# Optimization experiments

Measured on AMD Instinct MI355X. Metric: run time of the kernel, lower is better.

The kernel has to match this reference:

```python
import jax, jax.numpy as jnp
import numpy as np

N_S, N_G, D, K = 30000, 3000, 128, 16
SIGMA = 2.5
BOX = 60.0  # Angstrom box for random coordinates


def setup_inputs() -> dict:
    key = jax.random.key(0)
    ks = jax.random.split(key, 10)
    s = 1.0 / np.sqrt(D)
    return {
        'xs': jax.random.normal(ks[0], (N_S, D), jnp.float32),
        'xg': jax.random.normal(ks[1], (N_G, D), jnp.float32),
        'pos_s': jax.random.uniform(ks[2], (N_S, 3), jnp.float32) * BOX,
        'pos_g': jax.random.uniform(ks[3], (N_G, 3), jnp.float32) * BOX,
        'W_s_pre': jax.random.normal(ks[4], (D, D), jnp.float32) * s,
        'W_g_pre': jax.random.normal(ks[5], (D, D), jnp.float32) * s,
        'W_gs': jax.random.normal(ks[6], (D, D), jnp.float32) * s,
        'W_sg': jax.random.normal(ks[7], (D, D), jnp.float32) * s,
        'W_s_post': jax.random.normal(ks[8], (2 * D, D), jnp.float32) * s,
        'W_g_post': jax.random.normal(ks[9], (2 * D, D), jnp.float32) * s,
        'k': K,
    }


def reference(xs, xg, pos_s, pos_g, W_s_pre, W_g_pre, W_gs, W_sg, W_s_post, W_g_post, k):
    n_s, d = xs.shape
    # ---- compute_bipartite_graphs: knn of each graph node over surface nodes ----
    # squared pairwise distances via gemm form: (N_G, N_S)
    d2 = ((pos_g ** 2).sum(-1)[:, None] + (pos_s ** 2).sum(-1)[None, :]
          - 2.0 * pos_g @ pos_s.T)
    neg_d2, idx = jax.lax.top_k(-d2, k)          # idx: (N_G, K) surface neighbors
    w = jnp.exp(neg_d2 / (2.0 * SIGMA ** 2))     # RBF edge weight exp(-d^2/(2*sigma^2))
    # ---- pre blocks ----
    hs = xs @ W_s_pre                             # (N_S, D)
    hg = xg @ W_g_pre                             # (N_G, D)
    # ---- bp_gs block: graph -> surface weighted edge-conv (scatter-add) ----
    msg_gs = (hg @ W_gs)[:, None, :] * w[:, :, None]          # (N_G, K, D)
    xs_out = jnp.zeros((n_s, d), hs.dtype).at[idx.reshape(-1)].add(
        msg_gs.reshape(-1, d))
    # ---- bp_sg block: surface -> graph weighted edge-conv (gather-sum) ----
    xg_out = ((hs @ W_sg)[idx] * w[:, :, None]).sum(axis=1)   # (N_G, D)
    # ---- post blocks: combine pre features with message output ----
    xs_new = jax.nn.relu(jnp.concatenate([hs, xs_out], axis=-1) @ W_s_post)
    xg_new = jax.nn.relu(jnp.concatenate([hg, xg_out], axis=-1) @ W_g_post)
    return xs_new, xg_new
```

## Files before the change

### kernel.cpp

```cpp
#include <hip/hip_runtime.h>
#include <stdint.h>

#define N_S 30000
#define N_G 3000
#define DD  128
#define KK  16
#define NE  (N_G * KK)
#define NC  16
#define CELLS (NC * NC * NC)
#define CH  3.75f
#define CAP 16
#define SURV 192

#define FILL_BLOCKS 118
#define PACK_BLOCKS 384
#define KNN_BLOCKS  3000
#define NBS16 1875
#define NBG16 188
#define PRE_TILES (NBS16 + NBG16)
#define NBS 469
#define NBG 47
#define NTILE (NBS + NBG)

using v8s = __attribute__((ext_vector_type(8))) short;
using v4f = __attribute__((ext_vector_type(4))) float;

__device__ __forceinline__ float bf2f(unsigned short u) {
    union { unsigned int i; float f; } v; v.i = ((unsigned int)u) << 16; return v.f;
}
__device__ __forceinline__ unsigned short f2bf(float f) {
    union { float f; unsigned int i; } v; v.f = f;
    unsigned int x = v.i;
    return (unsigned short)((x + 0x7fffu + ((x >> 16) & 1u)) >> 16);
}
__device__ __forceinline__ float ldIn(const void* p, int i, int bf) {
    return bf ? bf2f(((const unsigned short*)p)[i]) : ((const float*)p)[i];
}
__device__ __forceinline__ void stOut(void* p, int i, float v, int bf) {
    if (bf) ((unsigned short*)p)[i] = f2bf(v);
    else    ((float*)p)[i] = v;
}
__device__ __forceinline__ int cellOf(float x) {
    int c = (int)(x * (1.0f / CH));
    if (c < 0) c = 0; if (c > NC - 1) c = NC - 1;
    return c;
}

__device__ __forceinline__ int detectFlag(const void* pos_g) {
    const unsigned int* w = (const unsigned int*)pos_g;
    int votes = 0;
#pragma unroll
    for (int i = 0; i < 16; ++i) {
        const unsigned int b = (w[i] >> 8) & 0xFFu;
        votes += (b >= 0x3Eu && b <= 0x42u) ? 1 : 0;
    }
    return votes >= 8;
}

__device__ bool knn_fast(int g, int bf, const void* pos_g,
                         const int* __restrict__ ccnt,
                         const float4* __restrict__ scell,
                         const float4* __restrict__ ovf, int novf,
                         int* __restrict__ idx_out, float* __restrict__ w_out,
                         double* skey, int* ssid)
{
    const int t = threadIdx.x;

    const float gxf = ldIn(pos_g, 3 * g + 0, bf);
    const float gyf = ldIn(pos_g, 3 * g + 1, bf);
    const float gzf = ldIn(pos_g, 3 * g + 2, bf);
    const double gx = (double)gxf, gy = (double)gyf, gz = (double)gzf;
    const int cx = cellOf(gxf), cy = cellOf(gyf), cz = cellOf(gzf);

    double m = 1e300;
    if (cx - 1 > 0)      { double d = gx - (double)(cx - 1) * 3.75; if (d < m) m = d; }
    if (cx + 1 < NC - 1) { double d = (double)(cx + 2) * 3.75 - gx; if (d < m) m = d; }
    if (cy - 1 > 0)      { double d = gy - (double)(cy - 1) * 3.75; if (d < m) m = d; }
    if (cy + 1 < NC - 1) { double d = (double)(cy + 2) * 3.75 - gy; if (d < m) m = d; }
    if (cz - 1 > 0)      { double d = gz - (double)(cz - 1) * 3.75; if (d < m) m = d; }
    if (cz + 1 < NC - 1) { double d = (double)(cz + 2) * 3.75 - gz; if (d < m) m = d; }
    if (m < 0.0) m = 0.0;
    const double m2eff = (m < 1e299) ? m * m * (1.0 - 1e-12) : 1e300;

    int cnt = 0, base = 0;
    if (t < 54) {
        const int cell = t >> 1, h = t & 1;
        const int dx = cell / 9 - 1, dy = (cell / 3) % 3 - 1, dz = cell % 3 - 1;
        const int X = cx + dx, Y = cy + dy, Z = cz + dz;
        if (X >= 0 && X < NC && Y >= 0 && Y < NC && Z >= 0 && Z < NC) {
            const int cid = (X * NC + Y) * NC + Z;
            int c = ccnt[cid]; if (c > CAP) c = CAP;
            const int lo = h * 8;
            const int hi = (c < lo + 8) ? c : (lo + 8);
            cnt = (hi > lo) ? (hi - lo) : 0;
            base = cid * CAP + lo;
        }
    }

    double d2v[8]; int sv[8]; bool okv[8];
#pragma unroll
    for (int i = 0; i < 8; ++i) {
        okv[i] = false; d2v[i] = 0.0; sv[i] = 0;
        if (i < cnt) {
            const float4 cd = scell[base + i];
            const double ddx = gx - (double)cd.x;
            const double ddy = gy - (double)cd.y;
            const double ddz = gz - (double)cd.z;
            const double d2 = ddx * ddx + ddy * ddy + ddz * ddz;
            if (d2 < m2eff) { okv[i] = true; d2v[i] = d2; sv[i] = __float_as_int(cd.w); }
        }
    }
    int myc = 0;
#pragma unroll
    for (int i = 0; i < 8; ++i) myc += okv[i] ? 1 : 0;

    int incl = myc;
    for (int d = 1; d < 64; d <<= 1) {
        int v = __shfl_up(incl, d);
        if (t >= d) incl += v;
    }
    int total = __shfl(incl, 63);
    int pos = incl - myc;
#pragma unroll
    for (int i = 0; i < 8; ++i) {
        if (okv[i]) {
            if (pos < SURV) { skey[pos] = d2v[i]; ssid[pos] = sv[i]; }
            ++pos;
        }
    }

    for (int i0 = 0; i0 < novf; i0 += 64) {
        const int i = i0 + t;
        bool act = (i < novf);
        double d2 = 0.0; int sidx = 0;
        if (act) {
            const float4 cd = ovf[i];
            const double ddx = gx - (double)cd.x;
            const double ddy = gy - (double)cd.y;
            const double ddz = gz - (double)cd.z;
            d2 = ddx * ddx + ddy * ddy + ddz * ddz;
            sidx = __float_as_int(cd.w);
            act = (d2 < m2eff);
        }
        const unsigned long long b = __ballot(act);
        const int p2 = total + (int)__popcll(b & ((1ull << t) - 1ull));
        if (act && p2 < SURV) { skey[p2] = d2; ssid[p2] = sidx; }
        total += (int)__popcll(b);
    }

    if (total < KK || total > SURV) return false;
    __syncthreads();

    const int n = total;
    double ki[3]; int si[3]; int rk[3]; int nv = 0;
    for (int i = t; i < n && nv < 3; i += 64) {
        ki[nv] = skey[i]; si[nv] = ssid[i]; rk[nv] = 0; ++nv;
    }
    for (int j = 0; j < n; ++j) {
        const double kj = skey[j]; const int sj = ssid[j];
#pragma unroll
        for (int q = 0; q < 3; ++q)
            if (q < nv)
                rk[q] += ((kj < ki[q]) || (kj == ki[q] && sj < si[q])) ? 1 : 0;
    }
#pragma unroll
    for (int q = 0; q < 3; ++q) {
        if (q < nv && rk[q] < KK) {
            idx_out[g * KK + rk[q]] = si[q];
            w_out[g * KK + rk[q]] = expf((float)(-ki[q]) * (1.0f / 12.5f));
        }
    }
    return true;
}

__device__ void knn_node(int g, int bf, const void* pos_g,
                         const int* __restrict__ ccnt,
                         const float4* __restrict__ scell,
                         const float4* __restrict__ ovf, int novf,
                         int* __restrict__ idx_out, float* __restrict__ w_out,
                         unsigned short* map16, int* s_base, int* s_pref,
                         double* g_key, int* g_sid)
{
    const int t = threadIdx.x;

    const float gxf = ldIn(pos_g, 3 * g + 0, bf);
    const float gyf = ldIn(pos_g, 3 * g + 1, bf);
    const float gzf = ldIn(pos_g, 3 * g + 2, bf);
    const double gx = (double)gxf, gy = (double)gyf, gz = (double)gzf;
    const int cx = cellOf(gxf), cy = cellOf(gyf), cz = cellOf(gzf);

    double bk[KK]; int bi[KK];
#pragma unroll
    for (int j = 0; j < KK; ++j) { bk[j] = 1e300; bi[j] = 0x7fffffff; }

    for (int i = t; i < novf; i += 64) {
        const float4 cd = ovf[i];
        const double ddx = gx - (double)cd.x, ddy = gy - (double)cd.y, ddz = gz - (double)cd.z;
        const double d2 = ddx * ddx + ddy * ddy + ddz * ddz;
        const int sidx = __float_as_int(cd.w);
        if (d2 > bk[KK - 1] || (d2 == bk[KK - 1] && sidx > bi[KK - 1])) continue;
        double ck = d2; int ci2 = sidx;
#pragma unroll
        for (int j = 0; j < KK; ++j) {
            const bool less = (ck < bk[j]) || (ck == bk[j] && ci2 < bi[j]);
            const double nk = less ? ck : bk[j]; const int ni = less ? ci2 : bi[j];
            const double ok = less ? bk[j] : ck; const int oi = less ? bi[j] : ci2;
            bk[j] = nk; bi[j] = ni; ck = ok; ci2 = oi;
        }
    }

    double gk15 = 1e300;
    for (int R = 1; R <= NC; ++R) {
        const int S = 2 * R + 1;
        const int Scells = S * S * S;
        for (int cb = 0; cb < Scells; cb += 64) {
            const int ci = cb + t;
            int cnt = 0, base = 0;
            if (ci < Scells) {
                const int dz = ci % S - R;
                const int dy = (ci / S) % S - R;
                const int dx = ci / (S * S) - R;
                int ax = dx < 0 ? -dx : dx, ay = dy < 0 ? -dy : dy, az = dz < 0 ? -dz : dz;
                int cheb = ax > ay ? ax : ay; if (az > cheb) cheb = az;
                const bool want = (R == 1) ? true : (cheb == R);
                const int X = cx + dx, Y = cy + dy, Z = cz + dz;
                if (want && X >= 0 && X < NC && Y >= 0 && Y < NC && Z >= 0 && Z < NC) {
                    double m2c = 0.0;
                    {
                        const double lo = (double)X * 3.75, hi = lo + 3.75;
                        const double d = (gx < lo) ? (lo - gx) : ((gx > hi) ? (gx - hi) : 0.0);
                        m2c += d * d;
                    }
                    {
                        const double lo = (double)Y * 3.75, hi = lo + 3.75;
                        const double d = (gy < lo) ? (lo - gy) : ((gy > hi) ? (gy - hi) : 0.0);
                        m2c += d * d;
                    }
                    {
                        const double lo = (double)Z * 3.75, hi = lo + 3.75;
                        const double d = (gz < lo) ? (lo - gz) : ((gz > hi) ? (gz - hi) : 0.0);
                        m2c += d * d;
                    }
                    if (m2c <= gk15 * (1.0 + 1e-9) + 1e-300) {
                        const int cid = (X * NC + Y) * NC + Z;
                        int c = ccnt[cid]; if (c > CAP) c = CAP;
                        cnt = c; base = cid * CAP;
                    }
                }
            }
            int incl = cnt;
            for (int d = 1; d < 64; d <<= 1) {
                int v = __shfl_up(incl, d);
                if (t >= d) incl += v;
            }
            const int total = __shfl(incl, 63);
            const int pref = incl - cnt;
            s_base[t] = base; s_pref[t] = pref;
            for (int i = 0; i < cnt; ++i) map16[pref + i] = (unsigned short)t;
            __syncthreads();
            for (int pos = t; pos < total; pos += 64) {
                const int slot = map16[pos];
                const float4 cd = scell[s_base[slot] + (pos - s_pref[slot])];
                const double ddx = gx - (double)cd.x;
                const double ddy = gy - (double)cd.y;
                const double ddz = gz - (double)cd.z;
                const double d2 = ddx * ddx + ddy * ddy + ddz * ddz;
                const int sidx = __float_as_int(cd.w);
                if (d2 > bk[KK - 1]) continue;
                if (d2 == bk[KK - 1] && sidx > bi[KK - 1]) continue;
                double ck = d2; int ci2 = sidx;
#pragma unroll
                for (int j = 0; j < KK; ++j) {
                    const bool less = (ck < bk[j]) || (ck == bk[j] && ci2 < bi[j]);
                    const double nk = less ? ck : bk[j]; const int ni = less ? ci2 : bi[j];
                    const double ok = less ? bk[j] : ck; const int oi = less ? bi[j] : ci2;
                    bk[j] = nk; bi[j] = ni; ck = ok; ci2 = oi;
                }
            }
            __syncthreads();
        }
        for (int p = 0; p < KK; ++p) {
            double key = bk[0]; int sid = bi[0];
            for (int d = 1; d < 64; d <<= 1) {
                const double ok = __shfl_xor(key, d);
                const int    os = __shfl_xor(sid, d);
                if (ok < key || (ok == key && os < sid)) { key = ok; sid = os; }
            }
            if (t == 0) { g_key[p] = key; g_sid[p] = sid; }
            const bool win = (bk[0] == key) && (bi[0] == sid);
            if (win) {
#pragma unroll
                for (int j = 0; j < KK - 1; ++j) { bk[j] = bk[j + 1]; bi[j] = bi[j + 1]; }
                bk[KK - 1] = 1e300; bi[KK - 1] = 0x7fffffff;
            }
        }
        __syncthreads();
        gk15 = g_key[KK - 1];
        if (t == 0) {
#pragma unroll
            for (int j = 0; j < KK; ++j) { bk[j] = g_key[j]; bi[j] = g_sid[j]; }
        } else {
#pragma unroll
            for (int j = 0; j < KK; ++j) { bk[j] = 1e300; bi[j] = 0x7fffffff; }
        }
        __syncthreads();
        double m = 1e300;
        if (cx - R > 0)      { double d = gx - (double)(cx - R) * 3.75; if (d < m) m = d; }
        if (cx + R < NC - 1) { double d = (double)(cx + R + 1) * 3.75 - gx; if (d < m) m = d; }
        if (cy - R > 0)      { double d = gy - (double)(cy - R) * 3.75; if (d < m) m = d; }
        if (cy + R < NC - 1) { double d = (double)(cy + R + 1) * 3.75 - gy; if (d < m) m = d; }
        if (cz - R > 0)      { double d = gz - (double)(cz - R) * 3.75; if (d < m) m = d; }
        if (cz + R < NC - 1) { double d = (double)(cz + R + 1) * 3.75 - gz; if (d < m) m = d; }
        if (m < 0.0) m = 0.0;
        const double m2 = m * m * (1.0 - 1e-12);
        if (gk15 < m2) break;
    }

    if (t == 0) {
        for (int p = 0; p < KK; ++p) {
            idx_out[g * KK + p] = g_sid[p];
            w_out[g * KK + p] = expf((float)(-g_key[p]) * (1.0f / 12.5f));
        }
    }
}

__device__ __forceinline__ v8s loadA_bf16(const unsigned short* p) {
    return *(const v8s*)p;
}
__device__ __forceinline__ v8s loadA_f32v(const float* f) {
    const float4 a = *(const float4*)f;
    const float4 b = *(const float4*)(f + 4);
    v8s r;
    r[0] = (short)f2bf(a.x); r[1] = (short)f2bf(a.y);
    r[2] = (short)f2bf(a.z); r[3] = (short)f2bf(a.w);
    r[4] = (short)f2bf(b.x); r[5] = (short)f2bf(b.y);
    r[6] = (short)f2bf(b.z); r[7] = (short)f2bf(b.w);
    return r;
}
__device__ __forceinline__ v8s loadA_raw(const void* A, size_t off, int bf) {
    if (bf) return loadA_bf16((const unsigned short*)A + off);
    return loadA_f32v((const float*)A + off);
}

__device__ void pre_tile16(int task, int bf, const void* xs, const void* xg,
                           const unsigned short* __restrict__ wpk_ps,
                           const unsigned short* __restrict__ wpk_pg,
                           unsigned short* __restrict__ hsb,
                           unsigned short* __restrict__ hgb,
                           float* __restrict__ xs_agg)
{
    const void* A; const unsigned short* wpk; unsigned short* outp; int M, m0;
    const bool is_s = (task < NBS16);
    if (is_s) { A = xs; wpk = wpk_ps; outp = hsb; M = N_S; m0 = task * 16; }
    else      { A = xg; wpk = wpk_pg; outp = hgb; M = N_G; m0 = (task - NBS16) * 16; }

    const int lane = threadIdx.x;
    const int q = lane >> 4, lm = lane & 15;
    const int mrow = m0 + lm;
    const bool valid = (mrow < M);

    v4f acc[8];
#pragma unroll
    for (int t = 0; t < 8; ++t) acc[t] = {0.f, 0.f, 0.f, 0.f};
    for (int ks = 0; ks < 4; ++ks) {
        v8s a = {0,0,0,0,0,0,0,0};
        if (valid) a = loadA_raw(A, (size_t)mrow * 128 + ks * 32 + q * 8, bf);
        const unsigned short* wb = wpk + (size_t)(ks * 4 + q) * 128 * 8;
#pragma unroll
        for (int t = 0; t < 8; ++t) {
            const v8s bfr = *(const v8s*)(wb + (t * 16 + lm) * 8);
            acc[t] = __builtin_amdgcn_mfma_f32_16x16x32_bf16(a, bfr, acc[t], 0, 0, 0);
        }
    }
#pragma unroll
    for (int t = 0; t < 8; ++t)
#pragma unroll
        for (int r = 0; r < 4; ++r) {
            const int row = m0 + q * 4 + r;
            if (row < M) outp[(size_t)row * 128 + t * 16 + lm] = f2bf(acc[t][r]);
        }
    if (is_s) {
        float4* dst = (float4*)(xs_agg + (size_t)m0 * 128);
        const float4 z = make_float4(0.f, 0.f, 0.f, 0.f);
        for (int i = lane; i < 16 * 32; i += 64) dst[i] = z;
    }
}

__device__ void post_tile(int task, int bf,
                          const unsigned short* __restrict__ hsb,
                          const float* __restrict__ xs_agg,
                          const unsigned short* __restrict__ hgb,
                          const unsigned short* __restrict__ aggg,
                          const unsigned short* __restrict__ wpk_cs,
                          const unsigned short* __restrict__ wpk_cg,
                          void* out)
{
    const unsigned short* A1; const void* A2; int a2f32; const unsigned short* wpk;
    int M, m0, ooff;
    if (task < NBS) { A1 = hsb; A2 = xs_agg; a2f32 = 1; wpk = wpk_cs; M = N_S; m0 = task * 64; ooff = 0; }
    else { A1 = hgb; A2 = aggg; a2f32 = 0; wpk = wpk_cg; M = N_G; m0 = (task - NBS) * 64; ooff = N_S * DD; }

    const int wave = threadIdx.x >> 6, lane = threadIdx.x & 63;
    const int q = lane >> 4, lm = lane & 15;
    const int mb = m0 + wave * 16;
    const int mrow = mb + lm;
    const bool valid = (mrow < M);

    v4f acc[8];
#pragma unroll
    for (int t = 0; t < 8; ++t) acc[t] = {0.f, 0.f, 0.f, 0.f};
    for (int ks = 0; ks < 8; ++ks) {
        const int kk = ks * 32 + q * 8;
        v8s a = {0,0,0,0,0,0,0,0};
        if (valid) {
            if (kk < 128)      a = loadA_bf16(A1 + (size_t)mrow * 128 + kk);
            else if (a2f32)    a = loadA_f32v((const float*)A2 + (size_t)mrow * 128 + (kk - 128));
            else               a = loadA_bf16((const unsigned short*)A2 + (size_t)mrow * 128 + (kk - 128));
        }
        const unsigned short* wb = wpk + (size_t)(ks * 4 + q) * 128 * 8;
#pragma unroll
        for (int t = 0; t < 8; ++t) {
            const v8s bfr = *(const v8s*)(wb + (t * 16 + lm) * 8);
            acc[t] = __builtin_amdgcn_mfma_f32_16x16x32_bf16(a, bfr, acc[t], 0, 0, 0);
        }
    }
#pragma unroll
    for (int t = 0; t < 8; ++t)
#pragma unroll
        for (int r = 0; r < 4; ++r) {
            const int row = mb + q * 4 + r;
            if (row < M) {
                float v = acc[t][r];
                if (v < 0.f) v = 0.f;
                stOut(out, ooff + row * DD + t * 16 + lm, v, bf);
            }
        }
}

__global__ __launch_bounds__(256) void fill_pack_kernel(
    const void* pos_s, const void* pos_g,
    const void* Wsp, const void* Wgp, const void* Wgs, const void* Wsg,
    const void* Wspost, const void* Wgpost,
    int* __restrict__ ccnt, float4* __restrict__ scell,
    float4* __restrict__ ovf, int* __restrict__ novf,
    unsigned short* __restrict__ wpk_ps, unsigned short* __restrict__ wpk_pg,
    unsigned short* __restrict__ wpk_cs, unsigned short* __restrict__ wpk_cg)
{
    const int bf = detectFlag(pos_g);
    const int bid = blockIdx.x, tid = threadIdx.x;
    if (bid < FILL_BLOCKS) {
        const int p = bid * 256 + tid;
        if (p < N_S) {
            const float x = ldIn(pos_s, 3 * p + 0, bf);
            const float y = ldIn(pos_s, 3 * p + 1, bf);
            const float z = ldIn(pos_s, 3 * p + 2, bf);
            const int cid = (cellOf(x) * NC + cellOf(y)) * NC + cellOf(z);
            const int slot = atomicAdd(&ccnt[cid], 1);
            const float4 pt = make_float4(x, y, z, __int_as_float(p));
            if (slot < CAP) scell[cid * CAP + slot] = pt;
            else            ovf[atomicAdd(novf, 1)] = pt;
        }
        return;
    }
    __shared__ float rows[256];
    const int rt = bid - FILL_BLOCKS;
    const int half = tid >> 7, j = tid & 127;
    const int task = rt * 2 + half;
    float v; unsigned short* dst; int k;
    if (task < 128) { k = task; v = ldIn(Wsp, k * DD + j, bf); dst = wpk_ps; }
    else if (task < 256) { k = task - 128; v = ldIn(Wgp, k * DD + j, bf); dst = wpk_pg; }
    else {
        const int which_g = (task >= 512);
        const int r = which_g ? (task - 512) : (task - 256);
        const void* W1 = which_g ? Wsg : Wgs;
        const void* Wp = which_g ? Wgpost : Wspost;
        dst = which_g ? wpk_cg : wpk_cs;
        k = r;
        if (r < 128) v = ldIn(Wp, r * DD + j, bf);
        else {
            rows[half * 128 + j] = ldIn(W1, (r - 128) * DD + j, bf);
            __syncthreads();
            float acc = 0.f;
            for (int m = 0; m < DD; ++m)
                acc += rows[half * 128 + m] * ldIn(Wp, (DD + m) * DD + j, bf);
            v = acc;
        }
    }
    const int ks = k >> 5, q = (k >> 3) & 3, i = k & 7;
    dst[((ks * 4 + q) * 128 + j) * 8 + i] = f2bf(v);
}

__global__ __launch_bounds__(64) void knn_pre_kernel(
    const void* xs, const void* xg, const void* pos_g,
    const int* __restrict__ ccnt, const float4* __restrict__ scell,
    const float4* __restrict__ ovf, const int* __restrict__ novf,
    int* __restrict__ idx, float* __restrict__ w,
    const unsigned short* __restrict__ wpk_ps,
    const unsigned short* __restrict__ wpk_pg,
    unsigned short* __restrict__ hsb, unsigned short* __restrict__ hgb,
    float* __restrict__ xs_agg)
{
    const int bf = detectFlag(pos_g);
    const int bid = blockIdx.x;
    if (bid < KNN_BLOCKS) {
        __shared__ double skey[SURV];
        __shared__ int    ssid[SURV];
        const int nov = *novf;
        if (!knn_fast(bid, bf, pos_g, ccnt, scell, ovf, nov, idx, w, skey, ssid)) {
            __shared__ unsigned short map16[64 * CAP];
            __shared__ int s_base[64];
            __shared__ int s_pref[64];
            __shared__ double g_key[KK];
            __shared__ int g_sid[KK];
            __syncthreads();
            knn_node(bid, bf, pos_g, ccnt, scell, ovf, nov, idx, w,
                     map16, s_base, s_pref, g_key, g_sid);
        }
    } else {
        pre_tile16(bid - KNN_BLOCKS, bf, xs, xg, wpk_ps, wpk_pg, hsb, hgb, xs_agg);
    }
}

__global__ __launch_bounds__(256) void scatgath_kernel(
    const unsigned short* __restrict__ hsb, const unsigned short* __restrict__ hgb,
    const int* __restrict__ idx, const float* __restrict__ w,
    float* __restrict__ xs_agg, unsigned short* __restrict__ aggg)
{
    const int g = blockIdx.x;
    const int half = threadIdx.x >> 7, j = threadIdx.x & 127;
    if (half == 0) {
        const float m = bf2f(hgb[g * DD + j]);
#pragma unroll
        for (int k = 0; k < KK; ++k)
            atomicAdd(&xs_agg[(size_t)idx[g * KK + k] * DD + j], m * w[g * KK + k]);
    } else {
        float acc = 0.f;
#pragma unroll
        for (int k = 0; k < KK; ++k)
            acc += w[g * KK + k] * bf2f(hsb[(size_t)idx[g * KK + k] * DD + j]);
        aggg[g * DD + j] = f2bf(acc);
    }
}

__global__ __launch_bounds__(256) void mfma_post_kernel(
    const void* pos_g,
    const unsigned short* __restrict__ hsb, const float* __restrict__ xs_agg,
    const unsigned short* __restrict__ hgb, const unsigned short* __restrict__ aggg,
    const unsigned short* __restrict__ wpk_cs, const unsigned short* __restrict__ wpk_cg,
    void* out)
{
    const int bf = detectFlag(pos_g);
    post_tile(blockIdx.x, bf, hsb, xs_agg, hgb, aggg, wpk_cs, wpk_cg, out);
}

extern "C" void kernel_launch(void* const* d_in, const int* in_sizes, int n_in,
                              void* d_out, int out_size, void* d_ws, size_t ws_size,
                              hipStream_t stream)
{
    const void* xs       = d_in[0];
    const void* xg       = d_in[1];
    const void* pos_s    = d_in[2];
    const void* pos_g    = d_in[3];
    const void* W_s_pre  = d_in[4];
    const void* W_g_pre  = d_in[5];
    const void* W_gs     = d_in[6];
    const void* W_sg     = d_in[7];
    const void* W_s_post = d_in[8];
    const void* W_g_post = d_in[9];
    (void)in_sizes; (void)n_in; (void)out_size; (void)ws_size;

    char* ws = (char*)d_ws;
    size_t off_b = 0;
    auto alloc = [&](size_t bytes) -> void* {
        void* p = ws + off_b;
        off_b = (off_b + bytes + 255) & ~((size_t)255);
        return p;
    };
    unsigned short* hsb    = (unsigned short*)alloc((size_t)N_S * DD * 2);
    unsigned short* hgb    = (unsigned short*)alloc((size_t)N_G * DD * 2);
    unsigned short* aggg   = (unsigned short*)alloc((size_t)N_G * DD * 2);
    float*          xs_agg = (float*) alloc((size_t)N_S * DD * 4);
    unsigned short* wpk_ps = (unsigned short*)alloc((size_t)DD * DD * 2);
    unsigned short* wpk_pg = (unsigned short*)alloc((size_t)DD * DD * 2);
    unsigned short* wpk_cs = (unsigned short*)alloc((size_t)2 * DD * DD * 2);
    unsigned short* wpk_cg = (unsigned short*)alloc((size_t)2 * DD * DD * 2);
    int*            idx    = (int*)   alloc((size_t)NE * 4);
    float*          w      = (float*) alloc((size_t)NE * 4);
    int*            ccnt   = (int*)   alloc((size_t)CELLS * 4 + 4);
    int*            novf   = ccnt + CELLS;
    float4*         scell  = (float4*)alloc((size_t)CELLS * CAP * 16);
    float4*         ovf    = (float4*)alloc((size_t)N_S * 16);

    hipMemsetAsync(ccnt, 0, (size_t)CELLS * 4 + 4, stream);

    fill_pack_kernel<<<FILL_BLOCKS + PACK_BLOCKS, 256, 0, stream>>>(
        pos_s, pos_g, W_s_pre, W_g_pre, W_gs, W_sg, W_s_post, W_g_post,
        ccnt, scell, ovf, novf, wpk_ps, wpk_pg, wpk_cs, wpk_cg);

    knn_pre_kernel<<<KNN_BLOCKS + PRE_TILES, 64, 0, stream>>>(
        xs, xg, pos_g, ccnt, scell, ovf, novf, idx, w,
        wpk_ps, wpk_pg, hsb, hgb, xs_agg);

    scatgath_kernel<<<N_G, 256, 0, stream>>>(hsb, hgb, idx, w,
                                             xs_agg, aggg);

    mfma_post_kernel<<<NTILE, 256, 0, stream>>>(pos_g, hsb, xs_agg, hgb, aggg,
                                                wpk_cs, wpk_cg, d_out);
}
```

Before: 186.7 us.

## Pack four waves per block for knn and pre tiles with expanding-region search

```diff
diff --git a/kernel.cpp b/kernel.cpp
--- a/kernel.cpp
+++ b/kernel.cpp
@@ -10,14 +10,15 @@
 #define CELLS (NC * NC * NC)
 #define CH  3.75f
 #define CAP 16
-#define SURV 192
+#define SURV 320
 
 #define FILL_BLOCKS 118
 #define PACK_BLOCKS 384
-#define KNN_BLOCKS  3000
+#define NODE_BLOCKS 750
 #define NBS16 1875
 #define NBG16 188
 #define PRE_TILES (NBS16 + NBG16)
+#define PRE_BLOCKS 516
 #define NBS 469
 #define NBG 47
 #define NTILE (NBS + NBG)
@@ -57,80 +58,86 @@
     return votes >= 8;
 }
 
-__device__ bool knn_fast(int g, int bf, const void* pos_g,
-                         const int* __restrict__ ccnt,
-                         const float4* __restrict__ scell,
-                         const float4* __restrict__ ovf, int novf,
-                         int* __restrict__ idx_out, float* __restrict__ w_out,
-                         double* skey, int* ssid)
-{
-    const int t = threadIdx.x;
-
-    const float gxf = ldIn(pos_g, 3 * g + 0, bf);
-    const float gyf = ldIn(pos_g, 3 * g + 1, bf);
-    const float gzf = ldIn(pos_g, 3 * g + 2, bf);
-    const double gx = (double)gxf, gy = (double)gyf, gz = (double)gzf;
-    const int cx = cellOf(gxf), cy = cellOf(gyf), cz = cellOf(gzf);
-
+__device__ __forceinline__ double regionM2(double gx, double gy, double gz,
+                                           int cx, int cy, int cz, int R)
+{
     double m = 1e300;
-    if (cx - 1 > 0)      { double d = gx - (double)(cx - 1) * 3.75; if (d < m) m = d; }
-    if (cx + 1 < NC - 1) { double d = (double)(cx + 2) * 3.75 - gx; if (d < m) m = d; }
-    if (cy - 1 > 0)      { double d = gy - (double)(cy - 1) * 3.75; if (d < m) m = d; }
-    if (cy + 1 < NC - 1) { double d = (double)(cy + 2) * 3.75 - gy; if (d < m) m = d; }
-    if (cz - 1 > 0)      { double d = gz - (double)(cz - 1) * 3.75; if (d < m) m = d; }
-    if (cz + 1 < NC - 1) { double d = (double)(cz + 2) * 3.75 - gz; if (d < m) m = d; }
+    if (cx - R > 0)      { double d = gx - (double)(cx - R) * 3.75; if (d < m) m = d; }
+    if (cx + R < NC - 1) { double d = (double)(cx + R + 1) * 3.75 - gx; if (d < m) m = d; }
+    if (cy - R > 0)      { double d = gy - (double)(cy - R) * 3.75; if (d < m) m = d; }
+    if (cy + R < NC - 1) { double d = (double)(cy + R + 1) * 3.75 - gy; if (d < m) m = d; }
+    if (cz - R > 0)      { double d = gz - (double)(cz - R) * 3.75; if (d < m) m = d; }
+    if (cz + R < NC - 1) { double d = (double)(cz + R + 1) * 3.75 - gz; if (d < m) m = d; }
     if (m < 0.0) m = 0.0;
-    const double m2eff = (m < 1e299) ? m * m * (1.0 - 1e-12) : 1e300;
-
-    int cnt = 0, base = 0;
-    if (t < 54) {
-        const int cell = t >> 1, h = t & 1;
-        const int dx = cell / 9 - 1, dy = (cell / 3) % 3 - 1, dz = cell % 3 - 1;
-        const int X = cx + dx, Y = cy + dy, Z = cz + dz;
-        if (X >= 0 && X < NC && Y >= 0 && Y < NC && Z >= 0 && Z < NC) {
-            const int cid = (X * NC + Y) * NC + Z;
-            int c = ccnt[cid]; if (c > CAP) c = CAP;
-            const int lo = h * 8;
-            const int hi = (c < lo + 8) ? c : (lo + 8);
-            cnt = (hi > lo) ? (hi - lo) : 0;
-            base = cid * CAP + lo;
-        }
-    }
-
-    double d2v[8]; int sv[8]; bool okv[8];
-#pragma unroll
-    for (int i = 0; i < 8; ++i) {
-        okv[i] = false; d2v[i] = 0.0; sv[i] = 0;
-        if (i < cnt) {
-            const float4 cd = scell[base + i];
-            const double ddx = gx - (double)cd.x;
-            const double ddy = gy - (double)cd.y;
-            const double ddz = gz - (double)cd.z;
-            const double d2 = ddx * ddx + ddy * ddy + ddz * ddz;
-            if (d2 < m2eff) { okv[i] = true; d2v[i] = d2; sv[i] = __float_as_int(cd.w); }
-        }
-    }
-    int myc = 0;
-#pragma unroll
-    for (int i = 0; i < 8; ++i) myc += okv[i] ? 1 : 0;
-
-    int incl = myc;
-    for (int d = 1; d < 64; d <<= 1) {
-        int v = __shfl_up(incl, d);
-        if (t >= d) incl += v;
-    }
-    int total = __shfl(incl, 63);
-    int pos = incl - myc;
-#pragma unroll
-    for (int i = 0; i < 8; ++i) {
-        if (okv[i]) {
-            if (pos < SURV) { skey[pos] = d2v[i]; ssid[pos] = sv[i]; }
-            ++pos;
-        }
+    return (m < 1e299) ? m * m * (1.0 - 1e-12) : 1e300;
+}
+
+__device__ int scanRegion(int R, int lane,
+                          double gx, double gy, double gz,
+                          int cx, int cy, int cz, double m2eff,
+                          const int* __restrict__ ccnt,
+                          const float4* __restrict__ scell,
+                          const float4* __restrict__ ovf, int novf,
+                          double* __restrict__ skey, int* __restrict__ ssid)
+{
+    const int S = 2 * R + 1;
+    const int S3 = S * S * S;
+    int total = 0;
+
+    for (int base = 0; base < 2 * S3; base += 64) {
+        const int pt = base + lane;
+        int cnt = 0, cbase = 0;
+        if (pt < 2 * S3) {
+            const int cell = pt >> 1, h = pt & 1;
+            int dx, dy, dz;
+            if (R == 1) {
+                dx = cell / 9 - 1; dy = (cell / 3) % 3 - 1; dz = cell % 3 - 1;
+            } else {
+                dx = cell / (S * S) - R; dy = (cell / S) % S - R; dz = cell % S - R;
+            }
+            const int X = cx + dx, Y = cy + dy, Z = cz + dz;
+            if (X >= 0 && X < NC && Y >= 0 && Y < NC && Z >= 0 && Z < NC) {
+                const int cid = (X * NC + Y) * NC + Z;
+                int c = ccnt[cid]; if (c > CAP) c = CAP;
+                const int lo = h * 8;
+                const int hi = (c < lo + 8) ? c : (lo + 8);
+                cnt = (hi > lo) ? (hi - lo) : 0;
+                cbase = cid * CAP + lo;
+            }
+        }
+        double d2v[8]; int sv[8]; int okm = 0;
+#pragma unroll
+        for (int i = 0; i < 8; ++i) {
+            d2v[i] = 0.0; sv[i] = 0;
+            if (i < cnt) {
+                const float4 cd = scell[cbase + i];
+                const double ddx = gx - (double)cd.x;
+                const double ddy = gy - (double)cd.y;
+                const double ddz = gz - (double)cd.z;
+                const double d2 = ddx * ddx + ddy * ddy + ddz * ddz;
+                if (d2 < m2eff) { okm |= (1 << i); d2v[i] = d2; sv[i] = __float_as_int(cd.w); }
+            }
+        }
+        int myc = __popc(okm);
+        int incl = myc;
+        for (int d = 1; d < 64; d <<= 1) {
+            int v = __shfl_up(incl, d);
+            if (lane >= d) incl += v;
+        }
+        int pos = total + (incl - myc);
+        total += __shfl(incl, 63);
+#pragma unroll
+        for (int i = 0; i < 8; ++i) {
+            if (okm & (1 << i)) {
+                if (pos < SURV) { skey[pos] = d2v[i]; ssid[pos] = sv[i]; }
+                ++pos;
+            }
+        }
+        if (total > SURV) return total;
     }
 
     for (int i0 = 0; i0 < novf; i0 += 64) {
-        const int i = i0 + t;
+        const int i = i0 + lane;
         bool act = (i < novf);
         double d2 = 0.0; int sidx = 0;
         if (act) {
@@ -143,183 +150,106 @@
             act = (d2 < m2eff);
         }
         const unsigned long long b = __ballot(act);
-        const int p2 = total + (int)__popcll(b & ((1ull << t) - 1ull));
+        const int p2 = total + (int)__popcll(b & ((1ull << lane) - 1ull));
         if (act && p2 < SURV) { skey[p2] = d2; ssid[p2] = sidx; }
         total += (int)__popcll(b);
     }
-
-    if (total < KK || total > SURV) return false;
-    __syncthreads();
-
-    const int n = total;
-    double ki[3]; int si[3]; int rk[3]; int nv = 0;
-    for (int i = t; i < n && nv < 3; i += 64) {
-        ki[nv] = skey[i]; si[nv] = ssid[i]; rk[nv] = 0; ++nv;
-    }
-    for (int j = 0; j < n; ++j) {
-        const double kj = skey[j]; const int sj = ssid[j];
-#pragma unroll
-        for (int q = 0; q < 3; ++q)
-            if (q < nv)
-                rk[q] += ((kj < ki[q]) || (kj == ki[q] && sj < si[q])) ? 1 : 0;
-    }
-#pragma unroll
-    for (int q = 0; q < 3; ++q) {
-        if (q < nv && rk[q] < KK) {
-            idx_out[g * KK + rk[q]] = si[q];
-            w_out[g * KK + rk[q]] = expf((float)(-ki[q]) * (1.0f / 12.5f));
-        }
-    }
-    return true;
-}
-
-__device__ void knn_node(int g, int bf, const void* pos_g,
+    return total;
+}
+
+__attribute__((noinline))
+__device__ void knn_brute(int g, int lane, int bf,
+                          const void* pos_g, const void* pos_s,
+                          int* __restrict__ idx_out, float* __restrict__ w_out)
+{
+    const double gx = (double)ldIn(pos_g, 3 * g + 0, bf);
+    const double gy = (double)ldIn(pos_g, 3 * g + 1, bf);
+    const double gz = (double)ldIn(pos_g, 3 * g + 2, bf);
+
+    double bk[KK]; int bi[KK];
+#pragma unroll
+    for (int j = 0; j < KK; ++j) { bk[j] = 1e300; bi[j] = 0x7fffffff; }
+
+    for (int i = lane; i < N_S; i += 64) {
+        const double ddx = gx - (double)ldIn(pos_s, 3 * i + 0, bf);
+        const double ddy = gy - (double)ldIn(pos_s, 3 * i + 1, bf);
+        const double ddz = gz - (double)ldIn(pos_s, 3 * i + 2, bf);
+        const double d2 = ddx * ddx + ddy * ddy + ddz * ddz;
+        if (d2 > bk[KK - 1] || (d2 == bk[KK - 1] && i > bi[KK - 1])) continue;
+        double ck = d2; int ci2 = i;
+#pragma unroll
+        for (int j = 0; j < KK; ++j) {
+            const bool less = (ck < bk[j]) || (ck == bk[j] && ci2 < bi[j]);
+            const double nk = less ? ck : bk[j]; const int ni = less ? ci2 : bi[j];
+            const double ok = less ? bk[j] : ck; const int oi = less ? bi[j] : ci2;
+            bk[j] = nk; bi[j] = ni; ck = ok; ci2 = oi;
+        }
+    }
+    for (int p = 0; p < KK; ++p) {
+        double key = bk[0]; int sid = bi[0];
+        for (int d = 1; d < 64; d <<= 1) {
+            const double ok = __shfl_xor(key, d);
+            const int    os = __shfl_xor(sid, d);
+            if (ok < key || (ok == key && os < sid)) { key = ok; sid = os; }
+        }
+        const bool win = (bk[0] == key) && (bi[0] == sid);
+        if (win) {
+#pragma unroll
+            for (int j = 0; j < KK - 1; ++j) { bk[j] = bk[j + 1]; bi[j] = bi[j + 1]; }
+            bk[KK - 1] = 1e300; bi[KK - 1] = 0x7fffffff;
+        }
+        if (lane == 0) {
+            idx_out[g * KK + p] = sid;
+            w_out[g * KK + p] = expf((float)(-key) * (1.0f / 12.5f));
+        }
+    }
+}
+
+__device__ void knn_wave(int g, int lane, int bf,
+                         const void* pos_g, const void* pos_s,
                          const int* __restrict__ ccnt,
                          const float4* __restrict__ scell,
                          const float4* __restrict__ ovf, int novf,
                          int* __restrict__ idx_out, float* __restrict__ w_out,
-                         unsigned short* map16, int* s_base, int* s_pref,
-                         double* g_key, int* g_sid)
-{
-    const int t = threadIdx.x;
-
+                         double* __restrict__ skey, int* __restrict__ ssid)
+{
     const float gxf = ldIn(pos_g, 3 * g + 0, bf);
     const float gyf = ldIn(pos_g, 3 * g + 1, bf);
     const float gzf = ldIn(pos_g, 3 * g + 2, bf);
     const double gx = (double)gxf, gy = (double)gyf, gz = (double)gzf;
     const int cx = cellOf(gxf), cy = cellOf(gyf), cz = cellOf(gzf);
 
-    double bk[KK]; int bi[KK];
-#pragma unroll
-    for (int j = 0; j < KK; ++j) { bk[j] = 1e300; bi[j] = 0x7fffffff; }
-
-    for (int i = t; i < novf; i += 64) {
-        const float4 cd = ovf[i];
-        const double ddx = gx - (double)cd.x, ddy = gy - (double)cd.y, ddz = gz - (double)cd.z;
-        const double d2 = ddx * ddx + ddy * ddy + ddz * ddz;
-        const int sidx = __float_as_int(cd.w);
-        if (d2 > bk[KK - 1] || (d2 == bk[KK - 1] && sidx > bi[KK - 1])) continue;
-        double ck = d2; int ci2 = sidx;
-#pragma unroll
-        for (int j = 0; j < KK; ++j) {
-            const bool less = (ck < bk[j]) || (ck == bk[j] && ci2 < bi[j]);
-            const double nk = less ? ck : bk[j]; const int ni = less ? ci2 : bi[j];
-            const double ok = less ? bk[j] : ck; const int oi = less ? bi[j] : ci2;
-            bk[j] = nk; bi[j] = ni; ck = ok; ci2 = oi;
-        }
-    }
-
-    double gk15 = 1e300;
+    int total = 0;
     for (int R = 1; R <= NC; ++R) {
-        const int S = 2 * R + 1;
-        const int Scells = S * S * S;
-        for (int cb = 0; cb < Scells; cb += 64) {
-            const int ci = cb + t;
-            int cnt = 0, base = 0;
-            if (ci < Scells) {
-                const int dz = ci % S - R;
-                const int dy = (ci / S) % S - R;
-                const int dx = ci / (S * S) - R;
-                int ax = dx < 0 ? -dx : dx, ay = dy < 0 ? -dy : dy, az = dz < 0 ? -dz : dz;
-                int cheb = ax > ay ? ax : ay; if (az > cheb) cheb = az;
-                const bool want = (R == 1) ? true : (cheb == R);
-                const int X = cx + dx, Y = cy + dy, Z = cz + dz;
-                if (want && X >= 0 && X < NC && Y >= 0 && Y < NC && Z >= 0 && Z < NC) {
-                    double m2c = 0.0;
-                    {
-                        const double lo = (double)X * 3.75, hi = lo + 3.75;
-                        const double d = (gx < lo) ? (lo - gx) : ((gx > hi) ? (gx - hi) : 0.0);
-                        m2c += d * d;
-                    }
-                    {
-                        const double lo = (double)Y * 3.75, hi = lo + 3.75;
-                        const double d = (gy < lo) ? (lo - gy) : ((gy > hi) ? (gy - hi) : 0.0);
-                        m2c += d * d;
-                    }
-                    {
-                        const double lo = (double)Z * 3.75, hi = lo + 3.75;
-                        const double d = (gz < lo) ? (lo - gz) : ((gz > hi) ? (gz - hi) : 0.0);
-                        m2c += d * d;
-                    }
-                    if (m2c <= gk15 * (1.0 + 1e-9) + 1e-300) {
-                        const int cid = (X * NC + Y) * NC + Z;
-                        int c = ccnt[cid]; if (c > CAP) c = CAP;
-                        cnt = c; base = cid * CAP;
-                    }
-                }
-            }
-            int incl = cnt;
-            for (int d = 1; d < 64; d <<= 1) {
-                int v = __shfl_up(incl, d);
-                if (t >= d) incl += v;
-            }
-            const int total = __shfl(incl, 63);
-            const int pref = incl - cnt;
-            s_base[t] = base; s_pref[t] = pref;
-            for (int i = 0; i < cnt; ++i) map16[pref + i] = (unsigned short)t;
-            __syncthreads();
-            for (int pos = t; pos < total; pos += 64) {
-                const int slot = map16[pos];
-                const float4 cd = scell[s_base[slot] + (pos - s_pref[slot])];
-                const double ddx = gx - (double)cd.x;
-                const double ddy = gy - (double)cd.y;
-                const double ddz = gz - (double)cd.z;
-                const double d2 = ddx * ddx + ddy * ddy + ddz * ddz;
-                const int sidx = __float_as_int(cd.w);
-                if (d2 > bk[KK - 1]) continue;
-                if (d2 == bk[KK - 1] && sidx > bi[KK - 1]) continue;
-                double ck = d2; int ci2 = sidx;
-#pragma unroll
-                for (int j = 0; j < KK; ++j) {
-                    const bool less = (ck < bk[j]) || (ck == bk[j] && ci2 < bi[j]);
-                    const double nk = less ? ck : bk[j]; const int ni = less ? ci2 : bi[j];
-                    const double ok = less ? bk[j] : ck; const int oi = less ? bi[j] : ci2;
-                    bk[j] = nk; bi[j] = ni; ck = ok; ci2 = oi;
-                }
-            }
-            __syncthreads();
-        }
-        for (int p = 0; p < KK; ++p) {
-            double key = bk[0]; int sid = bi[0];
-            for (int d = 1; d < 64; d <<= 1) {
-                const double ok = __shfl_xor(key, d);
-                const int    os = __shfl_xor(sid, d);
-                if (ok < key || (ok == key && os < sid)) { key = ok; sid = os; }
-            }
-            if (t == 0) { g_key[p] = key; g_sid[p] = sid; }
-            const bool win = (bk[0] == key) && (bi[0] == sid);
-            if (win) {
-#pragma unroll
-                for (int j = 0; j < KK - 1; ++j) { bk[j] = bk[j + 1]; bi[j] = bi[j + 1]; }
-                bk[KK - 1] = 1e300; bi[KK - 1] = 0x7fffffff;
-            }
-        }
-        __syncthreads();
-        gk15 = g_key[KK - 1];
-        if (t == 0) {
-#pragma unroll
-            for (int j = 0; j < KK; ++j) { bk[j] = g_key[j]; bi[j] = g_sid[j]; }
-        } else {
-#pragma unroll
-            for (int j = 0; j < KK; ++j) { bk[j] = 1e300; bi[j] = 0x7fffffff; }
-        }
-        __syncthreads();
-        double m = 1e300;
-        if (cx - R > 0)      { double d = gx - (double)(cx - R) * 3.75; if (d < m) m = d; }
-        if (cx + R < NC - 1) { double d = (double)(cx + R + 1) * 3.75 - gx; if (d < m) m = d; }
-        if (cy - R > 0)      { double d = gy - (double)(cy - R) * 3.75; if (d < m) m = d; }
-        if (cy + R < NC - 1) { double d = (double)(cy + R + 1) * 3.75 - gy; if (d < m) m = d; }
-        if (cz - R > 0)      { double d = gz - (double)(cz - R) * 3.75; if (d < m) m = d; }
-        if (cz + R < NC - 1) { double d = (double)(cz + R + 1) * 3.75 - gz; if (d < m) m = d; }
-        if (m < 0.0) m = 0.0;
-        const double m2 = m * m * (1.0 - 1e-12);
-        if (gk15 < m2) break;
-    }
-
-    if (t == 0) {
-        for (int p = 0; p < KK; ++p) {
-            idx_out[g * KK + p] = g_sid[p];
-            w_out[g * KK + p] = expf((float)(-g_key[p]) * (1.0f / 12.5f));
+        const double m2eff = regionM2(gx, gy, gz, cx, cy, cz, R);
+        total = scanRegion(R, lane, gx, gy, gz, cx, cy, cz, m2eff,
+                           ccnt, scell, ovf, novf, skey, ssid);
+        if (total >= KK || total > SURV) break;
+    }
+    if (total < KK || total > SURV) {
+        knn_brute(g, lane, bf, pos_g, pos_s, idx_out, w_out);
+        return;
+    }
+
+    asm volatile("s_waitcnt lgkmcnt(0)" ::: "memory");
+
+    const int n = total;
+    double ki[5]; int si[5]; int rk[5]; int nv = 0;
+    for (int i = lane; i < n && nv < 5; i += 64) {
+        ki[nv] = skey[i]; si[nv] = ssid[i]; rk[nv] = 0; ++nv;
+    }
+    for (int j = 0; j < n; ++j) {
+        const double kj = skey[j]; const int sj = ssid[j];
+#pragma unroll
+        for (int q = 0; q < 5; ++q)
+            if (q < nv)
+                rk[q] += ((kj < ki[q]) || (kj == ki[q] && sj < si[q])) ? 1 : 0;
+    }
+#pragma unroll
+    for (int q = 0; q < 5; ++q) {
+        if (q < nv && rk[q] < KK) {
+            idx_out[g * KK + rk[q]] = si[q];
+            w_out[g * KK + rk[q]] = expf((float)(-ki[q]) * (1.0f / 12.5f));
         }
     }
 }
@@ -342,7 +272,7 @@
     return loadA_f32v((const float*)A + off);
 }
 
-__device__ void pre_tile16(int task, int bf, const void* xs, const void* xg,
+__device__ void pre_tile16(int task, int lane, int bf, const void* xs, const void* xg,
                            const unsigned short* __restrict__ wpk_ps,
                            const unsigned short* __restrict__ wpk_pg,
                            unsigned short* __restrict__ hsb,
@@ -354,7 +284,6 @@
     if (is_s) { A = xs; wpk = wpk_ps; outp = hsb; M = N_S; m0 = task * 16; }
     else      { A = xg; wpk = wpk_pg; outp = hgb; M = N_G; m0 = (task - NBS16) * 16; }
 
-    const int lane = threadIdx.x;
     const int q = lane >> 4, lm = lane & 15;
     const int mrow = m0 + lm;
     const bool valid = (mrow < M);
@@ -490,8 +419,8 @@
     dst[((ks * 4 + q) * 128 + j) * 8 + i] = f2bf(v);
 }
 
-__global__ __launch_bounds__(64) void knn_pre_kernel(
-    const void* xs, const void* xg, const void* pos_g,
+__global__ __launch_bounds__(256) void knn_pre_kernel(
+    const void* xs, const void* xg, const void* pos_s, const void* pos_g,
     const int* __restrict__ ccnt, const float4* __restrict__ scell,
     const float4* __restrict__ ovf, const int* __restrict__ novf,
     int* __restrict__ idx, float* __restrict__ w,
@@ -502,22 +431,18 @@
 {
     const int bf = detectFlag(pos_g);
     const int bid = blockIdx.x;
-    if (bid < KNN_BLOCKS) {
-        __shared__ double skey[SURV];
-        __shared__ int    ssid[SURV];
+    const int wave = threadIdx.x >> 6, lane = threadIdx.x & 63;
+    if (bid < NODE_BLOCKS) {
+        __shared__ double skey[4][SURV];
+        __shared__ int    ssid[4][SURV];
+        const int g = bid * 4 + wave;
         const int nov = *novf;
-        if (!knn_fast(bid, bf, pos_g, ccnt, scell, ovf, nov, idx, w, skey, ssid)) {
-            __shared__ unsigned short map16[64 * CAP];
-            __shared__ int s_base[64];
-            __shared__ int s_pref[64];
-            __shared__ double g_key[KK];
-            __shared__ int g_sid[KK];
-            __syncthreads();
-            knn_node(bid, bf, pos_g, ccnt, scell, ovf, nov, idx, w,
-                     map16, s_base, s_pref, g_key, g_sid);
-        }
+        knn_wave(g, lane, bf, pos_g, pos_s, ccnt, scell, ovf, nov,
+                 idx, w, skey[wave], ssid[wave]);
     } else {
-        pre_tile16(bid - KNN_BLOCKS, bf, xs, xg, wpk_ps, wpk_pg, hsb, hgb, xs_agg);
+        const int task = (bid - NODE_BLOCKS) * 4 + wave;
+        if (task < PRE_TILES)
+            pre_tile16(task, lane, bf, xs, xg, wpk_ps, wpk_pg, hsb, hgb, xs_agg);
     }
 }
 
@@ -597,8 +522,8 @@
         pos_s, pos_g, W_s_pre, W_g_pre, W_gs, W_sg, W_s_post, W_g_post,
         ccnt, scell, ovf, novf, wpk_ps, wpk_pg, wpk_cs, wpk_cg);
 
-    knn_pre_kernel<<<KNN_BLOCKS + PRE_TILES, 64, 0, stream>>>(
-        xs, xg, pos_g, ccnt, scell, ovf, novf, idx, w,
+    knn_pre_kernel<<<NODE_BLOCKS + PRE_BLOCKS, 256, 0, stream>>>(
+        xs, xg, pos_s, pos_g, ccnt, scell, ovf, novf, idx, w,
         wpk_ps, wpk_pg, hsb, hgb, xs_agg);
 
     scatgath_kernel<<<N_G, 256, 0, stream>>>(hsb, hgb, idx, w,
```

Measured after the change: 217.1 us. +16.3%, slower.
